# Performance work log

Measured on AMD Instinct MI355X. Metric: run time of the kernel, lower is better.

## Reference

```python
import jax, jax.numpy as jnp
import numpy as np

D_MODEL = 512
N_HEADS = 8
HEAD_DIM = D_MODEL // N_HEADS
D_FF = 2048
EPS = 1e-5


def layer_norm(x, gamma, beta):
    mu = jnp.mean(x, axis=-1, keepdims=True)
    var = jnp.mean((x - mu) ** 2, axis=-1, keepdims=True)
    return (x - mu) * jax.lax.rsqrt(var + EPS) * gamma + beta


def setup_inputs() -> dict:
    key = jax.random.key(0)
    ks = jax.random.split(key, 17)
    B, S = 2, 2048
    s_in = 1.0 / np.sqrt(D_MODEL)
    s_ff = 1.0 / np.sqrt(D_FF)
    return {
        "x": jax.random.normal(ks[0], (B, S, D_MODEL), jnp.float32),
        "Wq": jax.random.normal(ks[1], (D_MODEL, D_MODEL), jnp.float32) * s_in,
        "bq": jnp.zeros((D_MODEL,), jnp.float32),
        "Wk": jax.random.normal(ks[2], (D_MODEL, D_MODEL), jnp.float32) * s_in,
        "bk": jnp.zeros((D_MODEL,), jnp.float32),
        "Wv": jax.random.normal(ks[3], (D_MODEL, D_MODEL), jnp.float32) * s_in,
        "bv": jnp.zeros((D_MODEL,), jnp.float32),
        "Wo": jax.random.normal(ks[4], (D_MODEL, D_MODEL), jnp.float32) * s_in,
        "bo": jnp.zeros((D_MODEL,), jnp.float32),
        "W1": jax.random.normal(ks[5], (D_MODEL, D_FF), jnp.float32) * s_in,
        "b1": jnp.zeros((D_FF,), jnp.float32),
        "W2": jax.random.normal(ks[6], (D_FF, D_MODEL), jnp.float32) * s_ff,
        "b2": jnp.zeros((D_MODEL,), jnp.float32),
        "g1": jnp.ones((D_MODEL,), jnp.float32),
        "be1": jnp.zeros((D_MODEL,), jnp.float32),
        "g2": jnp.ones((D_MODEL,), jnp.float32),
        "be2": jnp.zeros((D_MODEL,), jnp.float32),
    }


def reference(x, Wq, bq, Wk, bk, Wv, bv, Wo, bo, W1, b1, W2, b2, g1, be1, g2, be2):
    B, S, _ = x.shape
    # projections + split heads -> [B, H, S, Dh]
    def heads(t):
        return t.reshape(B, S, N_HEADS, HEAD_DIM).transpose(0, 2, 1, 3)
    q = heads(x @ Wq + bq)
    k = heads(x @ Wk + bk)
    v = heads(x @ Wv + bv)
    # explicit scaled dot-product attention (full [B,H,S,S] scores as in source)
    scores = jnp.einsum('bhqd,bhkd->bhqk', q, k) / np.sqrt(HEAD_DIM).astype(np.float32)
    attn = jax.nn.softmax(scores, axis=-1)
    ctx = jnp.einsum('bhqk,bhkd->bhqd', attn, v)
    ctx = ctx.transpose(0, 2, 1, 3).reshape(B, S, D_MODEL)
    attn_out = ctx @ Wo + bo
    # post-norm residual 1
    h = layer_norm(x + attn_out, g1, be1)
    # FFN
    ff = jax.nn.relu(h @ W1 + b1) @ W2 + b2
    # post-norm residual 2
    return layer_norm(h + ff, g2, be2)
```

## Files before the change

kernel.cpp:

```cpp
#include <hip/hip_runtime.h>
#include <cmath>

#define D_MODEL 512
#define N_HEADS 8
#define HEAD_DIM 64
#define D_FF 2048
#define SEQ 2048
#define BATCH 2
#define MROWS (BATCH * SEQ)

typedef __attribute__((ext_vector_type(8))) short short8;
typedef __attribute__((ext_vector_type(4))) float float4v;
typedef unsigned short ushort_t;

static __device__ __forceinline__ ushort_t f2bf(float f) {
    union { float f; unsigned u; } v; v.f = f;
    unsigned r = (v.u + 0x7FFFu + ((v.u >> 16) & 1u)) >> 16;
    return (ushort_t)r;
}
static __device__ __forceinline__ ushort_t f2bf_trunc(float f) {
    union { float f; unsigned u; } v; v.f = f;
    return (ushort_t)(v.u >> 16);
}

static __device__ __forceinline__ void gload16(const void* g, void* l) {
    __builtin_amdgcn_global_load_lds(
        (__attribute__((address_space(1))) void*)(unsigned long long)g,
        (__attribute__((address_space(3))) void*)(unsigned)(unsigned long long)l,
        16, 0, 0);
}

__global__ __launch_bounds__(256) void prep_k(
    const float* __restrict__ x,
    const float* __restrict__ Wq, const float* __restrict__ Wk,
    const float* __restrict__ Wv, const float* __restrict__ Wo,
    const float* __restrict__ W1, const float* __restrict__ W2,
    ushort_t* __restrict__ xb,
    ushort_t* __restrict__ WqkvT, ushort_t* __restrict__ WoT,
    ushort_t* __restrict__ W1T, ushort_t* __restrict__ W2T)
{
    int tile = blockIdx.x;
    if (tile >= 3072) {
        int i = (tile - 3072) * 256 + threadIdx.x;
        float4 f = ((const float4*)x)[i];
        ushort4 o;
        o.x = f2bf(f.x); o.y = f2bf(f.y); o.z = f2bf(f.z); o.w = f2bf(f.w);
        ((ushort4*)xb)[i] = o;
        return;
    }
    const float* src; ushort_t* dst; int Kd, Nd, tloc;
    if (tile < 1024) {
        int wsel = tile >> 8; tloc = tile & 255; Kd = 512; Nd = 512;
        if (wsel == 0)      { src = Wq; dst = WqkvT; }
        else if (wsel == 1) { src = Wk; dst = WqkvT + (size_t)512 * 512; }
        else if (wsel == 2) { src = Wv; dst = WqkvT + (size_t)1024 * 512; }
        else                { src = Wo; dst = WoT; }
    } else if (tile < 2048) { tloc = tile - 1024; Kd = 512;  Nd = 2048; src = W1; dst = W1T; }
    else                    { tloc = tile - 2048; Kd = 2048; Nd = 512;  src = W2; dst = W2T; }
    int tn = Nd >> 5;
    int k0 = (tloc / tn) << 5, n0 = (tloc % tn) << 5;
    __shared__ float tl[32][33];
    int c = threadIdx.x & 31, r = threadIdx.x >> 5;
    #pragma unroll
    for (int i = 0; i < 4; ++i)
        tl[r + i * 8][c] = src[(size_t)(k0 + r + i * 8) * Nd + n0 + c];
    __syncthreads();
    #pragma unroll
    for (int i = 0; i < 4; ++i)
        dst[(size_t)(n0 + r + i * 8) * Kd + k0 + c] = f2bf(tl[c][r + i * 8]);
}

template <int MODE>
__global__ __launch_bounds__(256) void gemm_std_k(
    const ushort_t* __restrict__ A, const ushort_t* __restrict__ BT,
    const float* __restrict__ bias, void* __restrict__ Cv,
    int N, int K, int Klen, size_t zstride)
{
    __shared__ ushort_t As[64 * 128];
    __shared__ ushort_t Bs[128 * 128];

    const int t = threadIdx.x;
    const int w = t >> 6, lane = t & 63, l16 = lane & 15, quad = lane >> 4;
    const int m0 = blockIdx.y * 64;
    const int n0 = blockIdx.x * 128;
    const int kbase = blockIdx.z * Klen;
    const int mbase = (w >> 1) * 32;
    const int nbase = (w & 1) * 64;
    const int lrow = lane >> 4;
    const int lchunk = lane & 15;

    float4v acc[2][4];
    #pragma unroll
    for (int mt = 0; mt < 2; ++mt)
        #pragma unroll
        for (int nt = 0; nt < 4; ++nt)
            acc[mt][nt] = (float4v){0.f, 0.f, 0.f, 0.f};

    for (int ks = kbase; ks < kbase + Klen; ks += 128) {
        __syncthreads();
        for (int c = w; c < 16; c += 4) {
            int rl = c * 4 + lrow;
            gload16(A + (size_t)(m0 + rl) * K + ks + ((lchunk ^ (rl & 7)) << 3),
                    &As[c * 512]);
        }
        for (int c = w; c < 32; c += 4) {
            int rl = c * 4 + lrow;
            gload16(BT + (size_t)(n0 + rl) * K + ks + ((lchunk ^ (rl & 7)) << 3),
                    &Bs[c * 512]);
        }
        __syncthreads();

        #pragma unroll
        for (int co = 0; co < 4; ++co) {
            const int poff = (((co * 4 + quad) ^ (l16 & 7)) << 3);
            short8 af[2], bf8[4];
            #pragma unroll
            for (int mt = 0; mt < 2; ++mt)
                af[mt] = *(const short8*)&As[(mbase + mt * 16 + l16) * 128 + poff];
            #pragma unroll
            for (int nt = 0; nt < 4; ++nt)
                bf8[nt] = *(const short8*)&Bs[(nbase + nt * 16 + l16) * 128 + poff];
            #pragma unroll
            for (int mt = 0; mt < 2; ++mt)
                #pragma unroll
                for (int nt = 0; nt < 4; ++nt)
                    acc[mt][nt] = __builtin_amdgcn_mfma_f32_16x16x32_bf16(
                        af[mt], bf8[nt], acc[mt][nt], 0, 0, 0);
        }
    }

    float* Cf = (float*)Cv + blockIdx.z * zstride;
    #pragma unroll
    for (int mt = 0; mt < 2; ++mt) {
        #pragma unroll
        for (int nt = 0; nt < 4; ++nt) {
            int gcol = n0 + nbase + nt * 16 + l16;
            float b = (MODE == 2) ? 0.f : bias[gcol];
            #pragma unroll
            for (int r = 0; r < 4; ++r) {
                int grow = m0 + mbase + mt * 16 + quad * 4 + r;
                float v = acc[mt][nt][r] + b;
                if (MODE == 1) v = fmaxf(v, 0.f);
                if (MODE == 1) ((ushort_t*)Cv)[(size_t)grow * N + gcol] = f2bf(v);
                else           Cf[(size_t)grow * N + gcol] = v;
            }
        }
    }
}

__global__ __launch_bounds__(256) void gemm_qkv_k(
    const ushort_t* __restrict__ A, const ushort_t* __restrict__ BT,
    const float* __restrict__ bq, const float* __restrict__ bk,
    const float* __restrict__ bv,
    ushort_t* __restrict__ Qb, ushort_t* __restrict__ Kb,
    ushort_t* __restrict__ VTb)
{
    __shared__ ushort_t As[64 * 128];
    __shared__ ushort_t Bs[128 * 128];

    const int t = threadIdx.x;
    const int w = t >> 6, lane = t & 63, l16 = lane & 15, quad = lane >> 4;
    const int m0 = blockIdx.y * 64;
    const int n0 = blockIdx.x * 128;
    const int mbase = (w >> 1) * 32;
    const int nbase = (w & 1) * 64;
    const int lrow = lane >> 4;
    const int lchunk = lane & 15;
    const int K = 512;

    float4v acc[2][4];
    #pragma unroll
    for (int mt = 0; mt < 2; ++mt)
        #pragma unroll
        for (int nt = 0; nt < 4; ++nt)
            acc[mt][nt] = (float4v){0.f, 0.f, 0.f, 0.f};

    for (int ks = 0; ks < 512; ks += 128) {
        __syncthreads();
        for (int c = w; c < 16; c += 4) {
            int rl = c * 4 + lrow;
            gload16(A + (size_t)(m0 + rl) * K + ks + ((lchunk ^ (rl & 7)) << 3),
                    &As[c * 512]);
        }
        for (int c = w; c < 32; c += 4) {
            int rl = c * 4 + lrow;
            gload16(BT + (size_t)(n0 + rl) * K + ks + ((lchunk ^ (rl & 7)) << 3),
                    &Bs[c * 512]);
        }
        __syncthreads();

        #pragma unroll
        for (int co = 0; co < 4; ++co) {
            const int poff = (((co * 4 + quad) ^ (l16 & 7)) << 3);
            short8 af[2], bf8[4];
            #pragma unroll
            for (int mt = 0; mt < 2; ++mt)
                af[mt] = *(const short8*)&As[(mbase + mt * 16 + l16) * 128 + poff];
            #pragma unroll
            for (int nt = 0; nt < 4; ++nt)
                bf8[nt] = *(const short8*)&Bs[(nbase + nt * 16 + l16) * 128 + poff];
            #pragma unroll
            for (int mt = 0; mt < 2; ++mt)
                #pragma unroll
                for (int nt = 0; nt < 4; ++nt)
                    acc[mt][nt] = __builtin_amdgcn_mfma_f32_16x16x32_bf16(
                        af[mt], bf8[nt], acc[mt][nt], 0, 0, 0);
        }
    }

    const int tsel = n0 >> 9;
    const float* bias = (tsel == 0) ? bq : (tsel == 1) ? bk : bv;
    const float scl = (tsel == 0) ? 0.18033688f : 1.0f;
    ushort_t* dst = (tsel == 0) ? Qb : Kb;

    #pragma unroll
    for (int mt = 0; mt < 2; ++mt) {
        #pragma unroll
        for (int nt = 0; nt < 4; ++nt) {
            int gcol = n0 + nbase + nt * 16 + l16;
            int lcol = gcol - (tsel << 9);
            int h = lcol >> 6, dh = lcol & 63;
            float b = bias[lcol];
            #pragma unroll
            for (int r = 0; r < 4; ++r) {
                int grow = m0 + mbase + mt * 16 + quad * 4 + r;
                int bb = grow >> 11, s = grow & 2047;
                float v = (acc[mt][nt][r] + b) * scl;
                if (tsel < 2)
                    dst[(((size_t)(bb * N_HEADS + h)) * SEQ + s) * HEAD_DIM + dh] = f2bf(v);
                else
                    VTb[(((size_t)(bb * N_HEADS + h)) * HEAD_DIM + dh) * SEQ + s] = f2bf(v);
            }
        }
    }
}

__global__ __launch_bounds__(256) void attn_mfma_k(
    const ushort_t* __restrict__ Qg, const ushort_t* __restrict__ Kg,
    const ushort_t* __restrict__ VTg,
    float* __restrict__ Opart, float* __restrict__ Lpart)
{
    __shared__ __align__(16) ushort_t Kbuf[2][64 * 64];
    __shared__ __align__(16) ushort_t Vbuf[2][64 * 64];
    __shared__ __align__(16) ushort_t Ps[4][16 * 64];

    const int bh = blockIdx.x;
    const int q0 = blockIdx.y * 64;
    const int ks = blockIdx.z;
    const int t = threadIdx.x;
    const int w = t >> 6;
    const int lane = t & 63;
    const int l16 = lane & 15;
    const int quad = lane >> 4;
    const int qbase = q0 + w * 16;
    const float M2 = 14.4269504f;

    const int r0 = t >> 3;
    const int r1 = r0 + 32;
    const int g0 = (t & 7) ^ (r0 & 7);
    const int g1 = (t & 7) ^ (r1 & 7);
    const size_t kgrow = (size_t)bh * SEQ;
    const size_t vgrow = (size_t)bh * HEAD_DIM;

#define ATTN_STAGE(b, kb)                                                       \
    {                                                                           \
        gload16(Kg + (kgrow + (kb) + r0) * HEAD_DIM + g0 * 8, &Kbuf[b][w * 512]);          \
        gload16(Kg + (kgrow + (kb) + r1) * HEAD_DIM + g1 * 8, &Kbuf[b][2048 + w * 512]);   \
        gload16(VTg + (vgrow + r0) * SEQ + (kb) + g0 * 8, &Vbuf[b][w * 512]);              \
        gload16(VTg + (vgrow + r1) * SEQ + (kb) + g1 * 8, &Vbuf[b][2048 + w * 512]);       \
    }

    short8 aq[2];
    {
        const ushort_t* qp = Qg + ((size_t)bh * SEQ + qbase + l16) * HEAD_DIM + quad * 8;
        aq[0] = *(const short8*)(qp);
        aq[1] = *(const short8*)(qp + 32);
    }

    float4v o[4] = {};
    float l_acc[4] = {0.f, 0.f, 0.f, 0.f};

    ATTN_STAGE(0, ks * 1024)

    for (int kt = 0; kt < 16; ++kt) {
        const int cur = kt & 1;
        if (kt < 15) {
            ATTN_STAGE(cur ^ 1, ks * 1024 + (kt + 1) * 64)
            asm volatile("s_waitcnt vmcnt(4)" ::: "memory");
        } else {
            asm volatile("s_waitcnt vmcnt(0)" ::: "memory");
        }
        asm volatile("s_barrier" ::: "memory");

        const ushort_t* Kc = Kbuf[cur];
        const ushort_t* Vc = Vbuf[cur];

        float4v s[4];
        #pragma unroll
        for (int nt = 0; nt < 4; ++nt) s[nt] = (float4v){0.f, 0.f, 0.f, 0.f};
        #pragma unroll
        for (int c = 0; c < 2; ++c) {
            const int poff = (((c * 4 + quad) ^ (l16 & 7)) << 3);
            #pragma unroll
            for (int nt = 0; nt < 4; ++nt) {
                short8 bk8 = *(const short8*)&Kc[(nt * 16 + l16) * 64 + poff];
                s[nt] = __builtin_amdgcn_mfma_f32_16x16x32_bf16(aq[c], bk8, s[nt], 0, 0, 0);
            }
        }

        #pragma unroll
        for (int nt = 0; nt < 4; ++nt) {
            #pragma unroll
            for (int r = 0; r < 4; ++r) {
                float p = exp2f(s[nt][r] - M2);
                s[nt][r] = p;
                l_acc[r] += p;
            }
        }

        #pragma unroll
        for (int nt = 0; nt < 4; ++nt)
            #pragma unroll
            for (int r = 0; r < 4; ++r) {
                int row = quad * 4 + r;
                int key = nt * 16 + l16;
                Ps[w][row * 64 + (((key >> 3) ^ (row & 7)) << 3) + (key & 7)] =
                    f2bf_trunc(s[nt][r]);
            }
        asm volatile("s_waitcnt lgkmcnt(0)" ::: "memory");

        #pragma unroll
        for (int c = 0; c < 2; ++c) {
            short8 ap = *(const short8*)&Ps[w][l16 * 64 + ((((c << 2) + quad) ^ (l16 & 7)) << 3)];
            const int poff = (((c * 4 + quad) ^ (l16 & 7)) << 3);
            #pragma unroll
            for (int dt = 0; dt < 4; ++dt) {
                short8 bv8 = *(const short8*)&Vc[(dt * 16 + l16) * 64 + poff];
                o[dt] = __builtin_amdgcn_mfma_f32_16x16x32_bf16(ap, bv8, o[dt], 0, 0, 0);
            }
        }

        asm volatile("s_barrier" ::: "memory");
    }
#undef ATTN_STAGE

    const size_t pbase = ((size_t)(ks * 16 + bh)) * SEQ;
    #pragma unroll
    for (int r = 0; r < 4; ++r) {
        float L = l_acc[r];
        #pragma unroll
        for (int msk = 1; msk < 16; msk <<= 1) L += __shfl_xor(L, msk);
        int qrow = qbase + quad * 4 + r;
        if (l16 == 0) Lpart[pbase + qrow] = L;
        #pragma unroll
        for (int dt = 0; dt < 4; ++dt)
            Opart[(pbase + qrow) * HEAD_DIM + dt * 16 + l16] = o[dt][r];
    }
}

__global__ __launch_bounds__(256) void attn_comb_k(
    const float* __restrict__ Op, const float* __restrict__ Lp,
    ushort_t* __restrict__ ctx)
{
    int g = blockIdx.x * 256 + threadIdx.x;
    int d4 = g & 15;
    int q  = (g >> 4) & 2047;
    int bh = g >> 15;
    float ax = 0.f, ay = 0.f, az = 0.f, aw = 0.f, L = 0.f;
    #pragma unroll
    for (int ks = 0; ks < 2; ++ks) {
        size_t row = ((size_t)(ks * 16 + bh) * SEQ + q) * HEAD_DIM;
        float4 a = ((const float4*)(Op + row))[d4];
        ax += a.x; ay += a.y; az += a.z; aw += a.w;
        L += Lp[ks * 16 * SEQ + bh * SEQ + q];
    }
    float inv = 1.0f / L;
    ushort4 o4;
    o4.x = f2bf(ax * inv);
    o4.y = f2bf(ay * inv);
    o4.z = f2bf(az * inv);
    o4.w = f2bf(aw * inv);
    int bb = bh >> 3, hh = bh & 7;
    *(ushort4*)&ctx[((size_t)(bb * SEQ + q)) * D_MODEL + hh * HEAD_DIM + d4 * 4] = o4;
}

template <int WRITE_BF>
__global__ __launch_bounds__(256) void add_ln_k(
    const float* __restrict__ X, const float* __restrict__ P0,
    const float* __restrict__ P1, const float* __restrict__ bias,
    const float* __restrict__ gam, const float* __restrict__ bet,
    float* __restrict__ O, ushort_t* __restrict__ Ob)
{
    const int row = blockIdx.x;
    const int t = threadIdx.x;
    const size_t ro = (size_t)row * D_MODEL;

    float v0 = X[ro + t]       + P0[ro + t]       + P1[ro + t]       + bias[t];
    float v1 = X[ro + t + 256] + P0[ro + t + 256] + P1[ro + t + 256] + bias[t + 256];
    float s = v0 + v1;
    float ss = v0 * v0 + v1 * v1;
    #pragma unroll
    for (int off = 32; off > 0; off >>= 1) {
        s  += __shfl_down(s, off);
        ss += __shfl_down(ss, off);
    }
    __shared__ float sb[4], ssb[4];
    if ((t & 63) == 0) { sb[t >> 6] = s; ssb[t >> 6] = ss; }
    __syncthreads();
    float S  = sb[0] + sb[1] + sb[2] + sb[3];
    float SS = ssb[0] + ssb[1] + ssb[2] + ssb[3];
    float mu  = S * (1.0f / D_MODEL);
    float var = SS * (1.0f / D_MODEL) - mu * mu;
    float inv = rsqrtf(var + 1e-5f);
    float o0 = (v0 - mu) * inv * gam[t] + bet[t];
    float o1 = (v1 - mu) * inv * gam[t + 256] + bet[t + 256];
    O[ro + t]       = o0;
    O[ro + t + 256] = o1;
    if (WRITE_BF) {
        Ob[ro + t]       = f2bf(o0);
        Ob[ro + t + 256] = f2bf(o1);
    }
}

extern "C" void kernel_launch(void* const* d_in, const int* in_sizes, int n_in,
                              void* d_out, int out_size, void* d_ws, size_t ws_size,
                              hipStream_t stream)
{
    const float* x   = (const float*)d_in[0];
    const float* Wq  = (const float*)d_in[1];
    const float* bq  = (const float*)d_in[2];
    const float* Wk  = (const float*)d_in[3];
    const float* bk  = (const float*)d_in[4];
    const float* Wv  = (const float*)d_in[5];
    const float* bv  = (const float*)d_in[6];
    const float* Wo  = (const float*)d_in[7];
    const float* bo  = (const float*)d_in[8];
    const float* W1  = (const float*)d_in[9];
    const float* b1  = (const float*)d_in[10];
    const float* W2  = (const float*)d_in[11];
    const float* b2  = (const float*)d_in[12];
    const float* g1  = (const float*)d_in[13];
    const float* be1 = (const float*)d_in[14];
    const float* g2  = (const float*)d_in[15];
    const float* be2 = (const float*)d_in[16];
    float* out = (float*)d_out;
    float* ws  = (float*)d_ws;

    ushort_t* WoT   = (ushort_t*)(ws);
    ushort_t* W1T   = (ushort_t*)(ws + 131072);
    ushort_t* W2T   = (ushort_t*)(ws + 655360);
    ushort_t* WqkvT = (ushort_t*)(ws + 1179648);
    ushort_t* xb    = (ushort_t*)(ws + 1572864);
    ushort_t* Qb    = (ushort_t*)(ws + 2621440);
    ushort_t* Kb    = (ushort_t*)(ws + 3670016);
    ushort_t* VTb   = (ushort_t*)(ws + 4718592);
    ushort_t* Ctx   = (ushort_t*)(ws + 5767168);
    float*    Lpart = ws + 6815744;
    float*    Hh    = ws + 6881280;
    float*    P0    = ws + 8978432;
    float*    P1    = ws + 11075584;
    float*    Opart = ws + 8978432;
    ushort_t* FF1   = (ushort_t*)(ws + 1572864);
    ushort_t* Hhb   = (ushort_t*)(ws + 5767168);

    prep_k<<<5120, 256, 0, stream>>>(x, Wq, Wk, Wv, Wo, W1, W2, xb, WqkvT, WoT, W1T, W2T);

    gemm_qkv_k<<<dim3(12, 64), 256, 0, stream>>>(xb, WqkvT, bq, bk, bv, Qb, Kb, VTb);

    attn_mfma_k<<<dim3(16, 32, 2), 256, 0, stream>>>(Qb, Kb, VTb, Opart, Lpart);
    attn_comb_k<<<2048, 256, 0, stream>>>(Opart, Lpart, Ctx);

    gemm_std_k<2><<<dim3(4, 64, 2), 256, 0, stream>>>(
        Ctx, WoT, nullptr, P0, 512, 512, 256, (size_t)MROWS * D_MODEL);

    add_ln_k<1><<<4096, 256, 0, stream>>>(x, P0, P1, bo, g1, be1, Hh, Hhb);

    gemm_std_k<1><<<dim3(16, 64), 256, 0, stream>>>(
        Hhb, W1T, b1, FF1, 2048, 512, 512, 0);

    gemm_std_k<2><<<dim3(4, 64, 2), 256, 0, stream>>>(
        FF1, W2T, nullptr, P0, 512, 2048, 1024, (size_t)MROWS * D_MODEL);

    add_ln_k<0><<<4096, 256, 0, stream>>>(Hh, P0, P1, b2, g2, be2, out, (ushort_t*)nullptr);
}
```

Baseline: 221.1 us.

## Retile GEMMs to 128-row M tiles with K=32 steps and smaller LDS

The projection and FFN GEMMs now use 128-row M tiles with a K step of 32 instead of 64-row tiles with a K step of 128. The output-projection and W2 GEMMs become templated with a 64-wide N tile. LDS use drops sharply, which should allow more resident blocks, and each warp computes a larger 64-row register tile for more reuse. In exchange there are four times as many K iterations, each with two barriers, and the XOR swizzle is removed, so LDS reads may hit bank conflicts. The grids shrink, halving the block count for the QKV and W1 GEMMs.

```diff
diff --git a/kernel.cpp b/kernel.cpp
--- a/kernel.cpp
+++ b/kernel.cpp
@@ -70,70 +70,64 @@
         dst[(size_t)(n0 + r + i * 8) * Kd + k0 + c] = f2bf(tl[c][r + i * 8]);
 }
 
-template <int MODE>
+template <int BN, int NT, int MODE>
 __global__ __launch_bounds__(256) void gemm_std_k(
     const ushort_t* __restrict__ A, const ushort_t* __restrict__ BT,
     const float* __restrict__ bias, void* __restrict__ Cv,
     int N, int K, int Klen, size_t zstride)
 {
-    __shared__ ushort_t As[64 * 128];
-    __shared__ ushort_t Bs[128 * 128];
+    __shared__ ushort_t As[128 * 32];
+    __shared__ ushort_t Bs[BN * 32];
 
     const int t = threadIdx.x;
     const int w = t >> 6, lane = t & 63, l16 = lane & 15, quad = lane >> 4;
-    const int m0 = blockIdx.y * 64;
-    const int n0 = blockIdx.x * 128;
+    const int m0 = blockIdx.y * 128;
+    const int n0 = blockIdx.x * BN;
     const int kbase = blockIdx.z * Klen;
-    const int mbase = (w >> 1) * 32;
-    const int nbase = (w & 1) * 64;
-    const int lrow = lane >> 4;
-    const int lchunk = lane & 15;
-
-    float4v acc[2][4];
-    #pragma unroll
-    for (int mt = 0; mt < 2; ++mt)
-        #pragma unroll
-        for (int nt = 0; nt < 4; ++nt)
+    const int mbase = (w >> 1) * 64;
+    const int nbase = (w & 1) * (NT * 16);
+    const int srow = lane >> 2;
+    const int schk = (lane & 3) * 8;
+
+    float4v acc[4][NT];
+    #pragma unroll
+    for (int mt = 0; mt < 4; ++mt)
+        #pragma unroll
+        for (int nt = 0; nt < NT; ++nt)
             acc[mt][nt] = (float4v){0.f, 0.f, 0.f, 0.f};
 
-    for (int ks = kbase; ks < kbase + Klen; ks += 128) {
+    for (int ks = kbase; ks < kbase + Klen; ks += 32) {
         __syncthreads();
-        for (int c = w; c < 16; c += 4) {
-            int rl = c * 4 + lrow;
-            gload16(A + (size_t)(m0 + rl) * K + ks + ((lchunk ^ (rl & 7)) << 3),
-                    &As[c * 512]);
-        }
-        for (int c = w; c < 32; c += 4) {
-            int rl = c * 4 + lrow;
-            gload16(BT + (size_t)(n0 + rl) * K + ks + ((lchunk ^ (rl & 7)) << 3),
-                    &Bs[c * 512]);
-        }
+        #pragma unroll
+        for (int g = 0; g < 2; ++g)
+            gload16(A + (size_t)(m0 + g * 64 + w * 16 + srow) * K + ks + schk,
+                    &As[g * 2048 + w * 512]);
+        #pragma unroll
+        for (int g = 0; g < BN / 64; ++g)
+            gload16(BT + (size_t)(n0 + g * 64 + w * 16 + srow) * K + ks + schk,
+                    &Bs[g * 2048 + w * 512]);
         __syncthreads();
 
-        #pragma unroll
-        for (int co = 0; co < 4; ++co) {
-            const int poff = (((co * 4 + quad) ^ (l16 & 7)) << 3);
-            short8 af[2], bf8[4];
-            #pragma unroll
-            for (int mt = 0; mt < 2; ++mt)
-                af[mt] = *(const short8*)&As[(mbase + mt * 16 + l16) * 128 + poff];
-            #pragma unroll
-            for (int nt = 0; nt < 4; ++nt)
-                bf8[nt] = *(const short8*)&Bs[(nbase + nt * 16 + l16) * 128 + poff];
-            #pragma unroll
-            for (int mt = 0; mt < 2; ++mt)
-                #pragma unroll
-                for (int nt = 0; nt < 4; ++nt)
-                    acc[mt][nt] = __builtin_amdgcn_mfma_f32_16x16x32_bf16(
-                        af[mt], bf8[nt], acc[mt][nt], 0, 0, 0);
-        }
+        short8 af[4], bf8[NT];
+        #pragma unroll
+        for (int mt = 0; mt < 4; ++mt)
+            af[mt] = *(const short8*)&As[(mbase + mt * 16 + l16) * 32 + quad * 8];
+        #pragma unroll
+        for (int nt = 0; nt < NT; ++nt)
+            bf8[nt] = *(const short8*)&Bs[(nbase + nt * 16 + l16) * 32 + quad * 8];
+        #pragma unroll
+        for (int mt = 0; mt < 4; ++mt)
+            #pragma unroll
+            for (int nt = 0; nt < NT; ++nt)
+                acc[mt][nt] = __builtin_amdgcn_mfma_f32_16x16x32_bf16(
+                    af[mt], bf8[nt], acc[mt][nt], 0, 0, 0);
     }
 
     float* Cf = (float*)Cv + blockIdx.z * zstride;
     #pragma unroll
-    for (int mt = 0; mt < 2; ++mt) {
-        #pragma unroll
-        for (int nt = 0; nt < 4; ++nt) {
+    for (int mt = 0; mt < 4; ++mt) {
+        #pragma unroll
+        for (int nt = 0; nt < NT; ++nt) {
             int gcol = n0 + nbase + nt * 16 + l16;
             float b = (MODE == 2) ? 0.f : bias[gcol];
             #pragma unroll
@@ -155,57 +149,51 @@
     ushort_t* __restrict__ Qb, ushort_t* __restrict__ Kb,
     ushort_t* __restrict__ VTb)
 {
-    __shared__ ushort_t As[64 * 128];
-    __shared__ ushort_t Bs[128 * 128];
+    __shared__ ushort_t As[128 * 32];
+    __shared__ ushort_t Bs[128 * 32];
 
     const int t = threadIdx.x;
     const int w = t >> 6, lane = t & 63, l16 = lane & 15, quad = lane >> 4;
-    const int m0 = blockIdx.y * 64;
+    const int m0 = blockIdx.y * 128;
     const int n0 = blockIdx.x * 128;
-    const int mbase = (w >> 1) * 32;
+    const int mbase = (w >> 1) * 64;
     const int nbase = (w & 1) * 64;
-    const int lrow = lane >> 4;
-    const int lchunk = lane & 15;
+    const int srow = lane >> 2;
+    const int schk = (lane & 3) * 8;
     const int K = 512;
 
-    float4v acc[2][4];
-    #pragma unroll
-    for (int mt = 0; mt < 2; ++mt)
+    float4v acc[4][4];
+    #pragma unroll
+    for (int mt = 0; mt < 4; ++mt)
         #pragma unroll
         for (int nt = 0; nt < 4; ++nt)
             acc[mt][nt] = (float4v){0.f, 0.f, 0.f, 0.f};
 
-    for (int ks = 0; ks < 512; ks += 128) {
+    for (int ks = 0; ks < 512; ks += 32) {
         __syncthreads();
-        for (int c = w; c < 16; c += 4) {
-            int rl = c * 4 + lrow;
-            gload16(A + (size_t)(m0 + rl) * K + ks + ((lchunk ^ (rl & 7)) << 3),
-                    &As[c * 512]);
-        }
-        for (int c = w; c < 32; c += 4) {
-            int rl = c * 4 + lrow;
-            gload16(BT + (size_t)(n0 + rl) * K + ks + ((lchunk ^ (rl & 7)) << 3),
-                    &Bs[c * 512]);
-        }
+        #pragma unroll
+        for (int g = 0; g < 2; ++g)
+            gload16(A + (size_t)(m0 + g * 64 + w * 16 + srow) * K + ks + schk,
+                    &As[g * 2048 + w * 512]);
+        #pragma unroll
+        for (int g = 0; g < 2; ++g)
+            gload16(BT + (size_t)(n0 + g * 64 + w * 16 + srow) * K + ks + schk,
+                    &Bs[g * 2048 + w * 512]);
         __syncthreads();
 
-        #pragma unroll
-        for (int co = 0; co < 4; ++co) {
-            const int poff = (((co * 4 + quad) ^ (l16 & 7)) << 3);
-            short8 af[2], bf8[4];
-            #pragma unroll
-            for (int mt = 0; mt < 2; ++mt)
-                af[mt] = *(const short8*)&As[(mbase + mt * 16 + l16) * 128 + poff];
+        short8 af[4], bf8[4];
+        #pragma unroll
+        for (int mt = 0; mt < 4; ++mt)
+            af[mt] = *(const short8*)&As[(mbase + mt * 16 + l16) * 32 + quad * 8];
+        #pragma unroll
+        for (int nt = 0; nt < 4; ++nt)
+            bf8[nt] = *(const short8*)&Bs[(nbase + nt * 16 + l16) * 32 + quad * 8];
+        #pragma unroll
+        for (int mt = 0; mt < 4; ++mt)
             #pragma unroll
             for (int nt = 0; nt < 4; ++nt)
-                bf8[nt] = *(const short8*)&Bs[(nbase + nt * 16 + l16) * 128 + poff];
-            #pragma unroll
-            for (int mt = 0; mt < 2; ++mt)
-                #pragma unroll
-                for (int nt = 0; nt < 4; ++nt)
-                    acc[mt][nt] = __builtin_amdgcn_mfma_f32_16x16x32_bf16(
-                        af[mt], bf8[nt], acc[mt][nt], 0, 0, 0);
-        }
+                acc[mt][nt] = __builtin_amdgcn_mfma_f32_16x16x32_bf16(
+                    af[mt], bf8[nt], acc[mt][nt], 0, 0, 0);
     }
 
     const int tsel = n0 >> 9;
@@ -214,7 +202,7 @@
     ushort_t* dst = (tsel == 0) ? Qb : Kb;
 
     #pragma unroll
-    for (int mt = 0; mt < 2; ++mt) {
+    for (int mt = 0; mt < 4; ++mt) {
         #pragma unroll
         for (int nt = 0; nt < 4; ++nt) {
             int gcol = n0 + nbase + nt * 16 + l16;
@@ -465,20 +453,20 @@
 
     prep_k<<<5120, 256, 0, stream>>>(x, Wq, Wk, Wv, Wo, W1, W2, xb, WqkvT, WoT, W1T, W2T);
 
-    gemm_qkv_k<<<dim3(12, 64), 256, 0, stream>>>(xb, WqkvT, bq, bk, bv, Qb, Kb, VTb);
+    gemm_qkv_k<<<dim3(12, 32), 256, 0, stream>>>(xb, WqkvT, bq, bk, bv, Qb, Kb, VTb);
 
     attn_mfma_k<<<dim3(16, 32, 2), 256, 0, stream>>>(Qb, Kb, VTb, Opart, Lpart);
     attn_comb_k<<<2048, 256, 0, stream>>>(Opart, Lpart, Ctx);
 
-    gemm_std_k<2><<<dim3(4, 64, 2), 256, 0, stream>>>(
+    gemm_std_k<64, 2, 2><<<dim3(8, 32, 2), 256, 0, stream>>>(
         Ctx, WoT, nullptr, P0, 512, 512, 256, (size_t)MROWS * D_MODEL);
 
     add_ln_k<1><<<4096, 256, 0, stream>>>(x, P0, P1, bo, g1, be1, Hh, Hhb);
 
-    gemm_std_k<1><<<dim3(16, 64), 256, 0, stream>>>(
+    gemm_std_k<128, 4, 1><<<dim3(16, 32), 256, 0, stream>>>(
         Hhb, W1T, b1, FF1, 2048, 512, 512, 0);
 
-    gemm_std_k<2><<<dim3(4, 64, 2), 256, 0, stream>>>(
+    gemm_std_k<64, 2, 2><<<dim3(8, 32, 2), 256, 0, stream>>>(
         FF1, W2T, nullptr, P0, 512, 2048, 1024, (size_t)MROWS * D_MODEL);
 
     add_ln_k<0><<<4096, 256, 0, stream>>>(Hh, P0, P1, b2, g2, be2, out, (ushort_t*)nullptr);
```

Result: slower. 229.1 us (+3.6%).
